# Kernel optimization log

Hardware: AMD Instinct MI355X
Metric: run time of the kernel (lower is better)

Reference implementation:

```python
import jax, jax.numpy as jnp
import numpy as np

HIDDEN = 51


def setup_inputs() -> dict:
    key = jax.random.key(0)
    ks = jax.random.split(key, 7)
    B, L = 1024, 1000
    inp = {
        "x": jax.random.normal(ks[0], (B, L), dtype=jnp.float32),
        "W_w": jax.random.normal(ks[1], (4 * HIDDEN, 1), dtype=jnp.float32) * 0.5,
        "W_b": jax.random.normal(ks[2], (4 * HIDDEN,), dtype=jnp.float32) * 0.1,
        "U_w": jax.random.normal(ks[3], (4 * HIDDEN, HIDDEN), dtype=jnp.float32) * 0.1,
        "U_b": jax.random.normal(ks[4], (4 * HIDDEN,), dtype=jnp.float32) * 0.1,
        "lin_w": jax.random.normal(ks[5], (1, HIDDEN), dtype=jnp.float32) * 0.1,
        "lin_b": jax.random.normal(ks[6], (1,), dtype=jnp.float32) * 0.1,
        "future": 0,
    }
    return inp


def _cell(x_t, h, c, W_w, W_b, U_w, U_b):
    # x_t: [B,1], h/c: [B,H]. NOTE: faithful to source, gates get NO
    # sigmoid/tanh; only c_t gets tanh before producing h_t.
    gates = x_t @ W_w.T + W_b + h @ U_w.T + U_b  # [B, 4H]
    i_t, f_t, g_t, o_t = jnp.split(gates, 4, axis=-1)
    c_t = f_t * c + i_t * g_t
    h_t = o_t * jnp.tanh(c_t)
    return h_t, c_t


def reference(x, W_w, W_b, U_w, U_b, lin_w, lin_b, future):
    B, L = x.shape
    h0 = jnp.zeros((B, HIDDEN), dtype=x.dtype)
    c0 = jnp.zeros((B, HIDDEN), dtype=x.dtype)

    def step(carry, x_t):
        h, c = carry
        h, c = _cell(x_t, h, c, W_w, W_b, U_w, U_b)
        out = h @ lin_w.T + lin_b  # [B,1]
        return (h, c), out

    xs = x.T[:, :, None]  # [L, B, 1]
    (h, c), outs = jax.lax.scan(step, (h0, c0), xs)
    outputs = [jnp.transpose(outs[:, :, 0])]  # [B, L]

    out = outs[-1]  # [B,1]
    fut = []
    for _ in range(future):
        h, c = _cell(out, h, c, W_w, W_b, U_w, U_b)
        out = h @ lin_w.T + lin_b
        fut.append(out[:, 0])
    if fut:
        outputs.append(jnp.stack(fut, axis=1))
    return jnp.concatenate(outputs, axis=1)  # [B, L+future]
```

## Files before the change

### kernel.cpp

```cpp
#include <hip/hip_runtime.h>

#define HIDDEN 51
#define LSEQ 1000
#define UNROLL 8

typedef _Float16 half2_t __attribute__((ext_vector_type(2)));

#if __has_builtin(__builtin_amdgcn_fdot2)
#define FDOT2(a, b, c) __builtin_amdgcn_fdot2((a), (b), (c), false)
#else
#define FDOT2(a, b, c) fmaf((float)(a).y, (float)(b).y, \
                       fmaf((float)(a).x, (float)(b).x, (c)))
#endif

__device__ __forceinline__ float fast_tanh(float v) {
    float e = __builtin_amdgcn_exp2f(v * 2.885390081777927f);
    float r = __builtin_amdgcn_rcpf(e + 1.0f);
    return fmaf(-2.0f, r, 1.0f);
}

__global__ __launch_bounds__(64, 1) void lstm_seq_kernel(
    const float* __restrict__ x,
    const float* __restrict__ W_w,
    const float* __restrict__ W_b,
    const float* __restrict__ U_w,
    const float* __restrict__ U_b,
    const float* __restrict__ lin_w,
    const float* __restrict__ lin_b,
    float* __restrict__ out)
{
    __shared__ __attribute__((aligned(16))) _Float16 hb16[64];

    const int b    = blockIdx.x;
    const int lane = threadIdx.x;
    const bool active = lane < HIDDEN;
    const int m = active ? lane : 0;

    float ww[4], bbias[4];
#pragma unroll
    for (int g = 0; g < 4; ++g) {
        const int row = m + g * HIDDEN;
        ww[g]    = active ? W_w[row] : 0.f;
        bbias[g] = active ? (W_b[row] + U_b[row]) : 0.f;
    }
    const float lw = active ? lin_w[m] : 0.f;
    const float lb = lin_b[0];

    half2_t Up[4][26];
#pragma unroll
    for (int j = 0; j < 26; ++j) {
        const int k0 = 2 * j, k1 = 2 * j + 1;
#pragma unroll
        for (int g = 0; g < 4; ++g) {
            const int row = m + g * HIDDEN;
            half2_t u;
            u.x = (_Float16)((active && k0 < HIDDEN) ? U_w[row * HIDDEN + k0] : 0.f);
            u.y = (_Float16)((active && k1 < HIDDEN) ? U_w[row * HIDDEN + k1] : 0.f);
            Up[g][j] = u;
        }
    }

    float h = 0.f, c = 0.f;
    const float* __restrict__ xrow = x + (long)b * LSEQ;
    float* __restrict__ orow = out + (long)b * LSEQ;

    hb16[lane] = (_Float16)0.f;
    __builtin_amdgcn_wave_barrier();

    const uint4* __restrict__ hbv = (const uint4*)hb16;

    for (int T = 0; T < LSEQ; T += UNROLL) {
        float xg[UNROLL], rb[UNROLL];
#pragma unroll
        for (int s = 0; s < UNROLL; ++s) xg[s] = xrow[T + s];

#pragma unroll
        for (int s = 0; s < UNROLL; ++s) {
            uint4 hq[7];
#pragma unroll
            for (int q = 0; q < 7; ++q) hq[q] = hbv[q];

            float a0 = fmaf(xg[s], ww[0], bbias[0]);
            float a1 = fmaf(xg[s], ww[1], bbias[1]);
            float a2 = fmaf(xg[s], ww[2], bbias[2]);
            float a3 = fmaf(xg[s], ww[3], bbias[3]);
#pragma unroll
            for (int q = 0; q < 7; ++q) {
                const unsigned int wds[4] = {hq[q].x, hq[q].y, hq[q].z, hq[q].w};
#pragma unroll
                for (int e = 0; e < 4; ++e) {
                    const int j = 4 * q + e;
                    if (j < 26) {
                        const half2_t hp = __builtin_bit_cast(half2_t, wds[e]);
                        a0 = FDOT2(hp, Up[0][j], a0);
                        a1 = FDOT2(hp, Up[1][j], a1);
                        a2 = FDOT2(hp, Up[2][j], a2);
                        a3 = FDOT2(hp, Up[3][j], a3);
                    }
                }
            }

            c = fmaf(a1, c, a0 * a2);
            h = a3 * fast_tanh(c);

            __builtin_amdgcn_wave_barrier();
            hb16[lane] = (_Float16)h;
            __builtin_amdgcn_wave_barrier();
            rb[s] = h * lw;
        }

#pragma unroll
        for (int s = 0; s < UNROLL; ++s) {
#pragma unroll
            for (int off = 32; off > 0; off >>= 1)
                rb[s] += __shfl_xor(rb[s], off, 64);
        }
        if (lane == 0) {
            float4 o0 = {rb[0] + lb, rb[1] + lb, rb[2] + lb, rb[3] + lb};
            float4 o1 = {rb[4] + lb, rb[5] + lb, rb[6] + lb, rb[7] + lb};
            *(float4*)&orow[T]     = o0;
            *(float4*)&orow[T + 4] = o1;
        }
    }
}

extern "C" void kernel_launch(void* const* d_in, const int* in_sizes, int n_in,
                              void* d_out, int out_size, void* d_ws, size_t ws_size,
                              hipStream_t stream) {
    const float* x     = (const float*)d_in[0];
    const float* W_w   = (const float*)d_in[1];
    const float* W_b   = (const float*)d_in[2];
    const float* U_w   = (const float*)d_in[3];
    const float* U_b   = (const float*)d_in[4];
    const float* lin_w = (const float*)d_in[5];
    const float* lin_b = (const float*)d_in[6];
    float* out = (float*)d_out;

    const int B = in_sizes[0] / LSEQ;
    lstm_seq_kernel<<<dim3(B), dim3(64), 0, stream>>>(
        x, W_w, W_b, U_w, U_b, lin_w, lin_b, out);
}
```

Before: 428.8 us.

## Use DPP row-shift reduction for output dot and prefetch next x chunk

Replaces the shfl_xor butterfly reduction of the output projection with a DPP-based reduction that accumulates into lane 63. Each reduction now runs inside the step loop, where it can overlap with the recurrent dependency chain. The x values for the next 8-step chunk are also loaded one iteration ahead to hide global-memory latency. The cost is extra per-step instructions on the serial critical path and a wasted prefetch on the final iteration.

```diff
diff --git a/kernel.cpp b/kernel.cpp
--- a/kernel.cpp
+++ b/kernel.cpp
@@ -17,6 +17,23 @@
     float e = __builtin_amdgcn_exp2f(v * 2.885390081777927f);
     float r = __builtin_amdgcn_rcpf(e + 1.0f);
     return fmaf(-2.0f, r, 1.0f);
+}
+
+template <int CTRL, int ROW_MASK>
+__device__ __forceinline__ float dpp_add(float v) {
+    int s = __builtin_amdgcn_update_dpp(0, __builtin_bit_cast(int, v),
+                                        CTRL, ROW_MASK, 0xf, true);
+    return v + __builtin_bit_cast(float, s);
+}
+
+__device__ __forceinline__ float wave_reduce_to63(float v) {
+    v = dpp_add<0x111, 0xf>(v);
+    v = dpp_add<0x112, 0xf>(v);
+    v = dpp_add<0x114, 0xf>(v);
+    v = dpp_add<0x118, 0xf>(v);
+    v = dpp_add<0x142, 0xa>(v);
+    v = dpp_add<0x143, 0xc>(v);
+    return v;
 }
 
 __global__ __launch_bounds__(64, 1) void lstm_seq_kernel(
@@ -69,11 +86,17 @@
 
     const uint4* __restrict__ hbv = (const uint4*)hb16;
 
+    float xg[UNROLL];
+#pragma unroll
+    for (int s = 0; s < UNROLL; ++s) xg[s] = xrow[s];
+
     for (int T = 0; T < LSEQ; T += UNROLL) {
-        float xg[UNROLL], rb[UNROLL];
+        const int Tn = (T + UNROLL < LSEQ) ? (T + UNROLL) : 0;
+        float xn[UNROLL];
 #pragma unroll
-        for (int s = 0; s < UNROLL; ++s) xg[s] = xrow[T + s];
+        for (int s = 0; s < UNROLL; ++s) xn[s] = xrow[Tn + s];
 
+        float rsum[UNROLL];
 #pragma unroll
         for (int s = 0; s < UNROLL; ++s) {
             uint4 hq[7];
@@ -106,21 +129,19 @@
             __builtin_amdgcn_wave_barrier();
             hb16[lane] = (_Float16)h;
             __builtin_amdgcn_wave_barrier();
-            rb[s] = h * lw;
+
+            rsum[s] = wave_reduce_to63(h * lw);
+        }
+
+        if (lane == 63) {
+            float4 o0 = {rsum[0] + lb, rsum[1] + lb, rsum[2] + lb, rsum[3] + lb};
+            float4 o1 = {rsum[4] + lb, rsum[5] + lb, rsum[6] + lb, rsum[7] + lb};
+            *(float4*)&orow[T]     = o0;
+            *(float4*)&orow[T + 4] = o1;
         }
 
 #pragma unroll
-        for (int s = 0; s < UNROLL; ++s) {
-#pragma unroll
-            for (int off = 32; off > 0; off >>= 1)
-                rb[s] += __shfl_xor(rb[s], off, 64);
-        }
-        if (lane == 0) {
-            float4 o0 = {rb[0] + lb, rb[1] + lb, rb[2] + lb, rb[3] + lb};
-            float4 o1 = {rb[4] + lb, rb[5] + lb, rb[6] + lb, rb[7] + lb};
-            *(float4*)&orow[T]     = o0;
-            *(float4*)&orow[T + 4] = o1;
-        }
+        for (int s = 0; s < UNROLL; ++s) xg[s] = xn[s];
     }
 }
 
```

Result: faster. 403.8 us (-5.8%).
